# Performance work log

Measured on AMD Instinct MI355X. Metric: run time of the kernel, lower is better.

## Reference

```python
import jax, jax.numpy as jnp
import numpy as np

B = 16
COUNTS = np.array([6, 14, 10, 8, 16, 12, 9, 11, 7, 13, 10, 10, 8, 12, 6, 8], dtype=np.int64)  # sum=160, max=16
INPUT_DIM = 1024
D_IN = 834   # num_features_mixed4f + 2
G = 256      # num_features_gcn
NG = 4       # num_graphs
T, H, W = 8, 14, 14


def setup_inputs() -> dict:
    key = jax.random.key(0)
    ks = jax.random.split(key, 7)
    total = int(COUNTS.sum())
    return {
        "actor_features": jax.random.normal(ks[0], (total, INPUT_DIM), dtype=jnp.float32),
        "feature_map": jax.random.normal(ks[1], (B, D_IN, T, H, W), dtype=jnp.float32),
        "W_a": jax.random.normal(ks[2], (NG, G, INPUT_DIM), dtype=jnp.float32) * 0.02,
        "b_a": jnp.zeros((NG, G), dtype=jnp.float32),
        "W_c": jax.random.normal(ks[3], (NG, G, D_IN), dtype=jnp.float32) * 0.02,
        "b_c": jnp.zeros((NG, G), dtype=jnp.float32),
        "W_h": jax.random.normal(ks[4], (NG, G, G), dtype=jnp.float32) * 0.02,
        "num_actors_list": COUNTS,
        "return_features": 0,
    }


def _ragged_indices(counts):
    # static (concrete) ragged bookkeeping
    counts = np.asarray(counts)
    Bn = counts.shape[0]
    Nmax = int(counts.max())
    offsets = np.concatenate([np.zeros(1, np.int64), np.cumsum(counts)[:-1]])
    n = np.arange(Nmax)
    pad_idx = offsets[:, None] + np.minimum(n[None, :], counts[:, None] - 1)  # [B, Nmax]
    valid = (n[None, :] < counts[:, None])                                     # [B, Nmax]
    unpad_b = np.repeat(np.arange(Bn), counts)
    unpad_n = np.concatenate([np.arange(c) for c in counts])
    return pad_idx, valid, unpad_b, unpad_n


def reference(actor_features, feature_map, W_a, b_a, W_c, b_c, W_h,
              num_actors_list, return_features):
    pad_idx, valid, unpad_b, unpad_n = _ragged_indices(num_actors_list)
    valid_f = jnp.asarray(valid, actor_features.dtype)
    Bn = feature_map.shape[0]

    # actor embedding for all graphs: [total, ng, G]
    emb = jnp.einsum('td,gfd->tgf', actor_features, W_a) + b_a[None]
    # pad to [B, Nmax, ng, G]; zero padded slots (matches pad_sequence)
    padded = emb[pad_idx] * valid_f[:, :, None, None]

    # 1x1x1 conv == channel matmul over flattened spatio-temporal grid S=T*H*W
    fm = feature_map.reshape(Bn, feature_map.shape[1], -1)            # [B, C, S]
    ctx = jnp.einsum('bcs,gfc->bgfs', fm, W_c) + b_c[None, :, :, None]  # [B, ng, G, S]

    # adjacency: actor x context similarities, softmax over context locations
    adj = jnp.einsum('bngf,bgfs->bgns', padded, ctx)                  # [B, ng, Nmax, S]
    adj = jax.nn.softmax(adj, axis=-1)
    adj = adj * valid_f[:, None, :, None]                             # masked_fill pad rows -> 0

    # aggregate context + residual
    upd = jnp.einsum('bgns,bgfs->bngf', adj, ctx) + padded            # [B, Nmax, ng, G]

    # unpad back to ragged flat [total, ng, G] (dropout is identity in eval)
    flat = upd[unpad_b, unpad_n]
    out = jax.nn.relu(jnp.einsum('tgf,ghf->tgh', flat, W_h))          # head_linear + relu

    # func == 'concat': cat over graphs along feature dim -> [total, ng*G]
    return out.reshape(out.shape[0], -1)
```

## Files before the change

### kernel.cpp

```cpp
#include <hip/hip_runtime.h>

#define TOTAL   160
#define NMAX    16
#define INDIM   1024
#define DIN     834
#define KPAD    864
#define GF      256
#define SS      1568
#define SPAD    1664
#define CROW    264

__constant__ int c_counts[16] = {6,14,10,8,16,12,9,11,7,13,10,10,8,12,6,8};
__constant__ int c_offs[16]   = {0,6,20,30,38,54,66,75,86,93,106,116,126,134,146,152};
__constant__ int c_t0[8] = {0, 6, 12, 18, 25, 31, 37, 43};
__constant__ int c_t1[8] = {6, 12, 18, 25, 31, 37, 43, 49};

using bf16x8 = __attribute__((ext_vector_type(8))) short;
using f32x4  = __attribute__((ext_vector_type(4))) float;
using us4    = __attribute__((ext_vector_type(4))) unsigned short;

__device__ inline unsigned short f2bf(float f) {
  union { float f; unsigned u; } v; v.f = f;
  const unsigned u = v.u;
  return (unsigned short)((u + 0x7FFFu + ((u >> 16) & 1u)) >> 16);
}
__device__ inline float bf2f(unsigned short h) {
  union { unsigned u; float f; } v; v.u = ((unsigned)h) << 16; return v.f;
}

__global__ __launch_bounds__(256) void prep_all(
    const float* __restrict__ actor, const float* __restrict__ Wa,
    const float* __restrict__ b_a, const float* __restrict__ Wc,
    const float* __restrict__ Wh, const float* __restrict__ fm,
    float* __restrict__ emb, unsigned short* __restrict__ emb_h,
    unsigned short* __restrict__ Ah, unsigned short* __restrict__ Wh_h,
    unsigned short* __restrict__ BhT)
{
  __shared__ float tile[32][33];
  __shared__ unsigned short As[64 * 40];
  __shared__ unsigned short Bs[64 * 40];
  const int bid = blockIdx.x, tid = threadIdx.x;

  if (bid < 48) {
    const int n0 = (bid & 15) * 64, m0 = (bid >> 4) * 64;
    const int wave = tid >> 6, lane = tid & 63;
    const int wm = (wave >> 1) * 32, wn = (wave & 1) * 32;
    const int quad = lane >> 4, lr = lane & 15;
    const int r = tid >> 2, ko = (tid & 3) * 8;
    const bool mval = (m0 + r < TOTAL);

    f32x4 acc[2][2];
    #pragma unroll
    for (int i = 0; i < 2; ++i)
      #pragma unroll
      for (int j = 0; j < 2; ++j) acc[i][j] = (f32x4){0.f, 0.f, 0.f, 0.f};

    const float4 zf4 = {0.f, 0.f, 0.f, 0.f};
    float4 ra0, ra1, rb0, rb1;
    ra0 = mval ? *reinterpret_cast<const float4*>(actor + (size_t)(m0 + r) * INDIM + ko) : zf4;
    ra1 = mval ? *reinterpret_cast<const float4*>(actor + (size_t)(m0 + r) * INDIM + ko + 4) : zf4;
    rb0 = *reinterpret_cast<const float4*>(Wa + (size_t)(n0 + r) * INDIM + ko);
    rb1 = *reinterpret_cast<const float4*>(Wa + (size_t)(n0 + r) * INDIM + ko + 4);

    for (int kt = 0; kt < 32; ++kt) {
      __syncthreads();
      {
        us4 a0, a1, b0, b1;
        a0[0]=f2bf(ra0.x); a0[1]=f2bf(ra0.y); a0[2]=f2bf(ra0.z); a0[3]=f2bf(ra0.w);
        a1[0]=f2bf(ra1.x); a1[1]=f2bf(ra1.y); a1[2]=f2bf(ra1.z); a1[3]=f2bf(ra1.w);
        b0[0]=f2bf(rb0.x); b0[1]=f2bf(rb0.y); b0[2]=f2bf(rb0.z); b0[3]=f2bf(rb0.w);
        b1[0]=f2bf(rb1.x); b1[1]=f2bf(rb1.y); b1[2]=f2bf(rb1.z); b1[3]=f2bf(rb1.w);
        *reinterpret_cast<us4*>(&As[r * 40 + ko])     = a0;
        *reinterpret_cast<us4*>(&As[r * 40 + ko + 4]) = a1;
        *reinterpret_cast<us4*>(&Bs[r * 40 + ko])     = b0;
        *reinterpret_cast<us4*>(&Bs[r * 40 + ko + 4]) = b1;
      }
      __syncthreads();
      if (kt < 31) {
        const int k0 = (kt + 1) * 32;
        ra0 = mval ? *reinterpret_cast<const float4*>(actor + (size_t)(m0 + r) * INDIM + k0 + ko) : zf4;
        ra1 = mval ? *reinterpret_cast<const float4*>(actor + (size_t)(m0 + r) * INDIM + k0 + ko + 4) : zf4;
        rb0 = *reinterpret_cast<const float4*>(Wa + (size_t)(n0 + r) * INDIM + k0 + ko);
        rb1 = *reinterpret_cast<const float4*>(Wa + (size_t)(n0 + r) * INDIM + k0 + ko + 4);
      }
      bf16x8 af[2], bfr[2];
      #pragma unroll
      for (int i = 0; i < 2; ++i)
        af[i] = *reinterpret_cast<const bf16x8*>(&As[(wm + i * 16 + lr) * 40 + quad * 8]);
      #pragma unroll
      for (int j = 0; j < 2; ++j)
        bfr[j] = *reinterpret_cast<const bf16x8*>(&Bs[(wn + j * 16 + lr) * 40 + quad * 8]);
      #pragma unroll
      for (int i = 0; i < 2; ++i)
        #pragma unroll
        for (int j = 0; j < 2; ++j)
          acc[i][j] = __builtin_amdgcn_mfma_f32_16x16x32_bf16(af[i], bfr[j], acc[i][j], 0, 0, 0);
    }

    #pragma unroll
    for (int i = 0; i < 2; ++i) {
      #pragma unroll
      for (int reg = 0; reg < 4; ++reg) {
        const int m = m0 + wm + i * 16 + quad * 4 + reg;
        if (m >= TOTAL) continue;
        #pragma unroll
        for (int j = 0; j < 2; ++j) {
          const int n = n0 + wn + j * 16 + lr;
          const float v = acc[i][j][reg] + b_a[n];
          emb[(size_t)m * INDIM + n] = v;
          emb_h[(size_t)m * INDIM + n] = f2bf(v);
        }
      }
    }
  } else if (bid < 3760) {
    const int pb = bid - 48;
    if (pb < 3456) {
      const int idx = pb * 256 + tid;
      const int k = idx % KPAD, gm = idx / KPAD;
      Ah[idx] = (k < DIN) ? f2bf(Wc[gm * DIN + k]) : (unsigned short)0;
    } else {
      const int i = (pb - 3456) * 256 + tid;
      const float4 v = reinterpret_cast<const float4*>(Wh)[i];
      us4 o; o[0] = f2bf(v.x); o[1] = f2bf(v.y); o[2] = f2bf(v.z); o[3] = f2bf(v.w);
      reinterpret_cast<us4*>(Wh_h)[i] = o;
    }
  } else {
    const int fb = bid - 3760;
    const int sx = fb % 49, ky = (fb / 49) % 27, b = fb / (49 * 27);
    const int k0 = ky * 32, s0 = sx * 32;
    const int tx = tid & 31, ty = tid >> 5;
    const float* src = fm + (size_t)b * DIN * SS;
    #pragma unroll
    for (int r = 0; r < 4; ++r) {
      const int k = k0 + ty + r * 8;
      tile[ty + r * 8][tx] = (k < DIN) ? src[(size_t)k * SS + s0 + tx] : 0.f;
    }
    __syncthreads();
    unsigned short* dst = BhT + (size_t)b * SS * KPAD;
    #pragma unroll
    for (int r = 0; r < 4; ++r) {
      const int s = s0 + ty + r * 8;
      dst[(size_t)s * KPAD + k0 + tx] = f2bf(tile[tx][ty + r * 8]);
    }
  }
}

#define CTX_STEP(RA0, RA1, RB0, RB1, KT)                                               \
  {                                                                                    \
    __syncthreads();                                                                   \
    *reinterpret_cast<uint4*>(&As[r0 * 40 + ko0]) = RA0;                               \
    *reinterpret_cast<uint4*>(&As[r1 * 40 + ko1]) = RA1;                               \
    *reinterpret_cast<uint4*>(&Bs[r0 * 40 + ko0]) = RB0;                               \
    *reinterpret_cast<uint4*>(&Bs[r1 * 40 + ko1]) = RB1;                               \
    __syncthreads();                                                                   \
    if ((KT) + 2 < 27) {                                                               \
      const int k0n = ((KT) + 2) * 32;                                                 \
      RA0 = *reinterpret_cast<const uint4*>(Ag + (size_t)(m0 + r0) * KPAD + k0n + ko0);\
      RA1 = *reinterpret_cast<const uint4*>(Ag + (size_t)(m0 + r1) * KPAD + k0n + ko1);\
      RB0 = *reinterpret_cast<const uint4*>(Bg + (size_t)r0 * KPAD + k0n + ko0);       \
      RB1 = *reinterpret_cast<const uint4*>(Bg + (size_t)r1 * KPAD + k0n + ko1);       \
    }                                                                                  \
    bf16x8 af[4], bfr[4];                                                              \
    _Pragma("unroll")                                                                  \
    for (int i = 0; i < 4; ++i)                                                        \
      af[i] = *reinterpret_cast<const bf16x8*>(&As[(wm + i * 16 + lr) * 40 + quad * 8]); \
    _Pragma("unroll")                                                                  \
    for (int j = 0; j < 4; ++j)                                                        \
      bfr[j] = *reinterpret_cast<const bf16x8*>(&Bs[(wn + j * 16 + lr) * 40 + quad * 8]); \
    _Pragma("unroll")                                                                  \
    for (int i = 0; i < 4; ++i)                                                        \
      _Pragma("unroll")                                                                \
      for (int j = 0; j < 4; ++j)                                                      \
        acc[i][j] = __builtin_amdgcn_mfma_f32_16x16x32_bf16(af[i], bfr[j], acc[i][j], 0, 0, 0); \
  }

__global__ __launch_bounds__(256, 3) void ctx_mfma(const unsigned short* __restrict__ Ah,
                                                   const unsigned short* __restrict__ BhT,
                                                   const float* __restrict__ b_c,
                                                   unsigned short* __restrict__ ctxT) {
  __shared__ unsigned short As[128 * 40];
  __shared__ unsigned short Bs[128 * 40];
  const int zb = blockIdx.z;
  const int g = zb & 3, b = zb >> 2;
  const int zout = (g << 4) + b;
  const int n0 = blockIdx.x * 128;
  const int m0 = blockIdx.y * 128;
  const int tid = threadIdx.x;
  const int wave = tid >> 6, lane = tid & 63;
  const int wm = (wave >> 1) * 64, wn = (wave & 1) * 64;
  const int quad = lane >> 4, lr = lane & 15;

  const unsigned short* Ag = BhT + (size_t)b * SS * KPAD;
  const unsigned short* Bg = Ah + (size_t)g * 256 * KPAD + (size_t)n0 * KPAD;

  const int c0 = tid, c1 = tid + 256;
  const int r0 = c0 >> 2, ko0 = (c0 & 3) * 8;
  const int r1 = c1 >> 2, ko1 = (c1 & 3) * 8;

  f32x4 acc[4][4];
  #pragma unroll
  for (int i = 0; i < 4; ++i)
    #pragma unroll
    for (int j = 0; j < 4; ++j) acc[i][j] = (f32x4){0.f, 0.f, 0.f, 0.f};

  uint4 ra0a, ra1a, rb0a, rb1a, ra0b, ra1b, rb0b, rb1b;
  ra0a = *reinterpret_cast<const uint4*>(Ag + (size_t)(m0 + r0) * KPAD + ko0);
  ra1a = *reinterpret_cast<const uint4*>(Ag + (size_t)(m0 + r1) * KPAD + ko1);
  rb0a = *reinterpret_cast<const uint4*>(Bg + (size_t)r0 * KPAD + ko0);
  rb1a = *reinterpret_cast<const uint4*>(Bg + (size_t)r1 * KPAD + ko1);
  ra0b = *reinterpret_cast<const uint4*>(Ag + (size_t)(m0 + r0) * KPAD + 32 + ko0);
  ra1b = *reinterpret_cast<const uint4*>(Ag + (size_t)(m0 + r1) * KPAD + 32 + ko1);
  rb0b = *reinterpret_cast<const uint4*>(Bg + (size_t)r0 * KPAD + 32 + ko0);
  rb1b = *reinterpret_cast<const uint4*>(Bg + (size_t)r1 * KPAD + 32 + ko1);

  for (int kt = 0; kt < 27; kt += 2) {
    CTX_STEP(ra0a, ra1a, rb0a, rb1a, kt);
    if (kt + 1 < 27) CTX_STEP(ra0b, ra1b, rb0b, rb1b, kt + 1);
  }

  unsigned short* Cz = ctxT + (size_t)zout * SPAD * GF;
  const float* bias = b_c + g * GF;
  #pragma unroll
  for (int j = 0; j < 4; ++j) {
    const int n = n0 + wn + j * 16 + lr;
    const float bv = bias[n];
    #pragma unroll
    for (int i = 0; i < 4; ++i) {
      #pragma unroll
      for (int reg = 0; reg < 4; ++reg) {
        const int m = m0 + wm + i * 16 + quad * 4 + reg;
        Cz[(size_t)m * GF + n] = f2bf(acc[i][j][reg] + bv);
      }
    }
  }
}

__global__ __launch_bounds__(256) void att_part(
    const unsigned short* __restrict__ ctxT,
    const unsigned short* __restrict__ emb_h,
    float* __restrict__ Opart,
    float* __restrict__ Spart)
{
  __shared__ unsigned short Cs[4][32 * CROW];
  __shared__ float Ps[4][32][20];
  __shared__ float walpha[4][16];
  __shared__ float wms[4][16], wls[4][16];
  const int sc = blockIdx.x, z = blockIdx.y;
  const int g = z >> 4, b = z & 15;
  const int count = c_counts[b], off = c_offs[b];
  const int t0 = c_t0[sc], t1 = c_t1[sc];
  const int tid = threadIdx.x, wave = tid >> 6, lane = tid & 63;
  const int quad = lane >> 4, lr = lane & 15;
  const unsigned short* Az = ctxT + (size_t)z * SPAD * GF;
  const bool bvalid = (lr < count);
  const unsigned short* Brow = emb_h + (size_t)(off + (bvalid ? lr : 0)) * INDIM + (g << 8);
  unsigned short* myC = &Cs[wave][0];
  const int fbase = quad * 64 + lr * 4;
  const bf16x8 zero8 = (bf16x8)(short)0;

  float O[16][4];
  #pragma unroll
  for (int n = 0; n < 16; ++n)
    #pragma unroll
    for (int j = 0; j < 4; ++j) O[n][j] = 0.f;
  float m_run = -3.0e38f, l_run = 0.f;

  for (int t = t0 + wave; t < t1; t += 4) {
    const int s0 = t * 32;
    #pragma unroll
    for (int q = 0; q < 16; ++q) {
      const int row = 2 * q + (lane >> 5);
      const int col = (lane & 31) * 8;
      const uint4 v = *reinterpret_cast<const uint4*>(Az + (size_t)(s0 + row) * GF + col);
      *reinterpret_cast<uint4*>(&myC[row * CROW + col]) = v;
    }
    f32x4 acc[2] = {(f32x4){0.f,0.f,0.f,0.f}, (f32x4){0.f,0.f,0.f,0.f}};
    #pragma unroll
    for (int kk = 0; kk < 8; ++kk) {
      const int f = kk * 32 + quad * 8;
      bf16x8 bv8 = *reinterpret_cast<const bf16x8*>(Brow + f);
      if (!bvalid) bv8 = zero8;
      #pragma unroll
      for (int i = 0; i < 2; ++i) {
        const bf16x8 av8 = *reinterpret_cast<const bf16x8*>(&myC[(i * 16 + lr) * CROW + f]);
        acc[i] = __builtin_amdgcn_mfma_f32_16x16x32_bf16(av8, bv8, acc[i], 0, 0, 0);
      }
    }
    float mx = acc[0][0];
    #pragma unroll
    for (int i = 0; i < 2; ++i)
      #pragma unroll
      for (int r = 0; r < 4; ++r) mx = fmaxf(mx, acc[i][r]);
    float lsum = 0.f;
    #pragma unroll
    for (int i = 0; i < 2; ++i)
      #pragma unroll
      for (int r = 0; r < 4; ++r) lsum += __expf(acc[i][r] - mx);
    #pragma unroll
    for (int d = 16; d < 64; d <<= 1) {
      const float om = __shfl_xor(mx, d, 64);
      const float ol = __shfl_xor(lsum, d, 64);
      const float M = fmaxf(mx, om);
      lsum = lsum * __expf(mx - M) + ol * __expf(om - M);
      mx = M;
    }
    const float m_new = fmaxf(m_run, mx);
    const float alpha = __expf(m_run - m_new);
    const float beta  = __expf(mx - m_new);
    l_run = alpha * l_run + beta * lsum;
    m_run = m_new;
    if (lane < 16) walpha[wave][lane] = alpha;
    #pragma unroll
    for (int i = 0; i < 2; ++i)
      #pragma unroll
      for (int r = 0; r < 4; ++r) {
        const int sl = i * 16 + quad * 4 + r;
        Ps[wave][sl][lr] = beta * __expf(acc[i][r] - mx);
      }
    float av[16];
    {
      const float4 a0 = *reinterpret_cast<const float4*>(&walpha[wave][0]);
      const float4 a1 = *reinterpret_cast<const float4*>(&walpha[wave][4]);
      const float4 a2 = *reinterpret_cast<const float4*>(&walpha[wave][8]);
      const float4 a3 = *reinterpret_cast<const float4*>(&walpha[wave][12]);
      av[0]=a0.x; av[1]=a0.y; av[2]=a0.z; av[3]=a0.w;
      av[4]=a1.x; av[5]=a1.y; av[6]=a1.z; av[7]=a1.w;
      av[8]=a2.x; av[9]=a2.y; av[10]=a2.z; av[11]=a2.w;
      av[12]=a3.x; av[13]=a3.y; av[14]=a3.z; av[15]=a3.w;
    }
    #pragma unroll
    for (int n = 0; n < 16; ++n)
      #pragma unroll
      for (int j = 0; j < 4; ++j) O[n][j] *= av[n];
    for (int s = 0; s < 32; ++s) {
      const float4 p0 = *reinterpret_cast<const float4*>(&Ps[wave][s][0]);
      const float4 p1 = *reinterpret_cast<const float4*>(&Ps[wave][s][4]);
      const float4 p2 = *reinterpret_cast<const float4*>(&Ps[wave][s][8]);
      const float4 p3 = *reinterpret_cast<const float4*>(&Ps[wave][s][12]);
      const us4 cv = *reinterpret_cast<const us4*>(&myC[s * CROW + fbase]);
      const float c0 = bf2f(cv[0]), c1 = bf2f(cv[1]), c2 = bf2f(cv[2]), c3 = bf2f(cv[3]);
      const float pn[16] = {p0.x,p0.y,p0.z,p0.w, p1.x,p1.y,p1.z,p1.w,
                            p2.x,p2.y,p2.z,p2.w, p3.x,p3.y,p3.z,p3.w};
      #pragma unroll
      for (int n = 0; n < 16; ++n) {
        O[n][0] = fmaf(pn[n], c0, O[n][0]);
        O[n][1] = fmaf(pn[n], c1, O[n][1]);
        O[n][2] = fmaf(pn[n], c2, O[n][2]);
        O[n][3] = fmaf(pn[n], c3, O[n][3]);
      }
    }
  }

  if (lane < 16) { wms[wave][lane] = m_run; wls[wave][lane] = l_run; }
  __syncthreads();
  float* Ob = reinterpret_cast<float*>(&Cs[wave][0]);
  #pragma unroll
  for (int n = 0; n < 16; ++n) {
    const float Mb = fmaxf(fmaxf(wms[0][n], wms[1][n]), fmaxf(wms[2][n], wms[3][n]));
    const float e = __expf(wms[wave][n] - Mb);
    #pragma unroll
    for (int j = 0; j < 4; ++j) Ob[n * 256 + fbase + j] = O[n][j] * e;
  }
  __syncthreads();
  float* Op = Opart + ((size_t)z * 8 + sc) * 4096;
  #pragma unroll
  for (int nn = 0; nn < 4; ++nn) {
    const int n = wave * 4 + nn;
    float4 v = {0.f, 0.f, 0.f, 0.f};
    #pragma unroll
    for (int w = 0; w < 4; ++w) {
      const float4 x = *reinterpret_cast<const float4*>(
          reinterpret_cast<const float*>(&Cs[w][0]) + n * 256 + fbase);
      v.x += x.x; v.y += x.y; v.z += x.z; v.w += x.w;
    }
    *reinterpret_cast<float4*>(Op + n * 256 + fbase) = v;
  }
  if (wave == 0 && lane < 16) {
    const int n = lane;
    const float Mb = fmaxf(fmaxf(wms[0][n], wms[1][n]), fmaxf(wms[2][n], wms[3][n]));
    float Lb = 0.f;
    #pragma unroll
    for (int w = 0; w < 4; ++w) Lb += wls[w][n] * __expf(wms[w][n] - Mb);
    Spart[((size_t)z * 8 + sc) * 32 + n]      = Mb;
    Spart[((size_t)z * 8 + sc) * 32 + 16 + n] = Lb;
  }
}

__global__ __launch_bounds__(256) void att_combine(
    const float* __restrict__ Opart, const float* __restrict__ Spart,
    const float* __restrict__ emb, unsigned short* __restrict__ flat_h) {
  const int z = blockIdx.x, n = blockIdx.y;
  const int g = z >> 4, b = z & 15;
  const int count = c_counts[b], off = c_offs[b];
  if (n >= count) return;
  const int f = threadIdx.x;
  float M = -3.0e38f;
  #pragma unroll
  for (int sc = 0; sc < 8; ++sc)
    M = fmaxf(M, Spart[((size_t)z * 8 + sc) * 32 + n]);
  float L = 0.f, acc = 0.f;
  #pragma unroll
  for (int sc = 0; sc < 8; ++sc) {
    const float e = __expf(Spart[((size_t)z * 8 + sc) * 32 + n] - M);
    L += e * Spart[((size_t)z * 8 + sc) * 32 + 16 + n];
    acc += e * Opart[((size_t)z * 8 + sc) * 4096 + n * 256 + f];
  }
  const int t = off + n;
  const int col = (g << 8) + f;
  flat_h[t * INDIM + col] = f2bf(acc / L + emb[t * INDIM + col]);
}

__global__ __launch_bounds__(256) void head_mfma(const unsigned short* __restrict__ flat_h,
                                                 const unsigned short* __restrict__ Wh_h,
                                                 float* __restrict__ out) {
  __shared__ unsigned short As[64 * 40];
  __shared__ unsigned short Bs[64 * 40];
  const int g = blockIdx.z;
  const int n0 = blockIdx.x * 64, m0 = blockIdx.y * 64;
  const int tid = threadIdx.x;
  const int wave = tid >> 6, lane = tid & 63;
  const int wm = (wave >> 1) * 32, wn = (wave & 1) * 32;
  const int quad = lane >> 4, lr = lane & 15;
  const int r = tid >> 2, ko = (tid & 3) * 8;

  const unsigned short* Ag = flat_h + (size_t)m0 * INDIM + g * GF;
  const unsigned short* Bg = Wh_h + (size_t)g * GF * GF + (size_t)n0 * GF;

  f32x4 acc[2][2];
  #pragma unroll
  for (int i = 0; i < 2; ++i)
    #pragma unroll
    for (int j = 0; j < 2; ++j) acc[i][j] = (f32x4){0.f, 0.f, 0.f, 0.f};

  const uint4 zero4 = {0u, 0u, 0u, 0u};
  uint4 ra, rb;
  ra = (m0 + r < TOTAL) ? *reinterpret_cast<const uint4*>(Ag + (size_t)r * INDIM + ko) : zero4;
  rb = *reinterpret_cast<const uint4*>(Bg + (size_t)r * GF + ko);

  for (int kt = 0; kt < 8; ++kt) {
    __syncthreads();
    *reinterpret_cast<uint4*>(&As[r * 40 + ko]) = ra;
    *reinterpret_cast<uint4*>(&Bs[r * 40 + ko]) = rb;
    __syncthreads();
    if (kt < 7) {
      const int k0 = (kt + 1) * 32;
      ra = (m0 + r < TOTAL) ? *reinterpret_cast<const uint4*>(Ag + (size_t)r * INDIM + k0 + ko) : zero4;
      rb = *reinterpret_cast<const uint4*>(Bg + (size_t)r * GF + k0 + ko);
    }
    bf16x8 af[2], bfr[2];
    #pragma unroll
    for (int i = 0; i < 2; ++i)
      af[i] = *reinterpret_cast<const bf16x8*>(&As[(wm + i * 16 + lr) * 40 + quad * 8]);
    #pragma unroll
    for (int j = 0; j < 2; ++j)
      bfr[j] = *reinterpret_cast<const bf16x8*>(&Bs[(wn + j * 16 + lr) * 40 + quad * 8]);
    #pragma unroll
    for (int i = 0; i < 2; ++i)
      #pragma unroll
      for (int j = 0; j < 2; ++j)
        acc[i][j] = __builtin_amdgcn_mfma_f32_16x16x32_bf16(af[i], bfr[j], acc[i][j], 0, 0, 0);
  }

  #pragma unroll
  for (int i = 0; i < 2; ++i) {
    #pragma unroll
    for (int reg = 0; reg < 4; ++reg) {
      const int m = m0 + wm + i * 16 + quad * 4 + reg;
      if (m >= TOTAL) continue;
      #pragma unroll
      for (int j = 0; j < 2; ++j) {
        const int n = n0 + wn + j * 16 + lr;
        out[(size_t)m * INDIM + g * GF + n] = fmaxf(acc[i][j][reg], 0.f);
      }
    }
  }
}

extern "C" void kernel_launch(void* const* d_in, const int* in_sizes, int n_in,
                              void* d_out, int out_size, void* d_ws, size_t ws_size,
                              hipStream_t stream) {
  (void)in_sizes; (void)n_in; (void)out_size; (void)ws_size;
  const float* actor = (const float*)d_in[0];
  const float* fmap  = (const float*)d_in[1];
  const float* W_a   = (const float*)d_in[2];
  const float* b_a   = (const float*)d_in[3];
  const float* W_c   = (const float*)d_in[4];
  const float* b_c   = (const float*)d_in[5];
  const float* W_h   = (const float*)d_in[6];
  float* out = (float*)d_out;
  char* ws = (char*)d_ws;

  float* emb             = (float*)(ws);
  unsigned short* flat_h = (unsigned short*)(ws + 655360);
  unsigned short* emb_h  = (unsigned short*)(ws + 983040);
  float* Spart           = (float*)(ws + 1310720);
  unsigned short* ctxT   = (unsigned short*)(ws + 1376256);
  unsigned short* Ah     = (unsigned short*)(ws + 55902208);
  unsigned short* BhT    = (unsigned short*)(ws + 57671680);
  float* Opart           = (float*)(ws + 57671680);
  unsigned short* Wh_h   = (unsigned short*)(ws + 101023744);

  hipLaunchKernelGGL(prep_all, dim3(24928), dim3(256), 0, stream,
                     actor, W_a, b_a, W_c, W_h, fmap,
                     emb, emb_h, Ah, Wh_h, BhT);

  hipLaunchKernelGGL(ctx_mfma, dim3(2, 13, 64), dim3(256), 0, stream, Ah, BhT, b_c, ctxT);

  hipLaunchKernelGGL(att_part, dim3(8, 64), dim3(256), 0, stream,
                     ctxT, emb_h, Opart, Spart);

  hipLaunchKernelGGL(att_combine, dim3(64, 16), dim3(256), 0, stream,
                     Opart, Spart, emb, flat_h);

  hipLaunchKernelGGL(head_mfma, dim3(4, 3, 4), dim3(256), 0, stream,
                     flat_h, Wh_h, out);
}
```

Baseline: 280.5 us.

## Use direct global-to-LDS loads and XCD-aware block mapping in ctx GEMM

The ctx GEMM now loads its A and B tiles with global_load_lds, which writes straight into shared memory instead of staging through registers. It also drops the register double-buffer prefetch and the padded LDS stride. The 3D grid becomes a 1D grid remapped so that each XCD handles two batches, keeping each batch's BhT slice in one XCD's L2. The trade-off is that loads no longer overlap compute within a block, and the unpadded 32-element LDS rows may cause bank conflicts on the fragment reads.

Result: faster. 265.4 us (-5.4%).

```diff
diff --git a/kernel.cpp b/kernel.cpp
--- a/kernel.cpp
+++ b/kernel.cpp
@@ -26,6 +26,12 @@
 }
 __device__ inline float bf2f(unsigned short h) {
   union { unsigned u; float f; } v; v.u = ((unsigned)h) << 16; return v.f;
+}
+
+__device__ __forceinline__ void gload16(const unsigned short* g, unsigned short* l) {
+  __builtin_amdgcn_global_load_lds(
+      (const __attribute__((address_space(1))) unsigned int*)(g),
+      (__attribute__((address_space(3))) unsigned int*)(l), 16, 0, 0);
 }
 
 __global__ __launch_bounds__(256) void prep_all(
@@ -145,57 +151,39 @@
   }
 }
 
-#define CTX_STEP(RA0, RA1, RB0, RB1, KT)                                               \
-  {                                                                                    \
-    __syncthreads();                                                                   \
-    *reinterpret_cast<uint4*>(&As[r0 * 40 + ko0]) = RA0;                               \
-    *reinterpret_cast<uint4*>(&As[r1 * 40 + ko1]) = RA1;                               \
-    *reinterpret_cast<uint4*>(&Bs[r0 * 40 + ko0]) = RB0;                               \
-    *reinterpret_cast<uint4*>(&Bs[r1 * 40 + ko1]) = RB1;                               \
-    __syncthreads();                                                                   \
-    if ((KT) + 2 < 27) {                                                               \
-      const int k0n = ((KT) + 2) * 32;                                                 \
-      RA0 = *reinterpret_cast<const uint4*>(Ag + (size_t)(m0 + r0) * KPAD + k0n + ko0);\
-      RA1 = *reinterpret_cast<const uint4*>(Ag + (size_t)(m0 + r1) * KPAD + k0n + ko1);\
-      RB0 = *reinterpret_cast<const uint4*>(Bg + (size_t)r0 * KPAD + k0n + ko0);       \
-      RB1 = *reinterpret_cast<const uint4*>(Bg + (size_t)r1 * KPAD + k0n + ko1);       \
-    }                                                                                  \
-    bf16x8 af[4], bfr[4];                                                              \
-    _Pragma("unroll")                                                                  \
-    for (int i = 0; i < 4; ++i)                                                        \
-      af[i] = *reinterpret_cast<const bf16x8*>(&As[(wm + i * 16 + lr) * 40 + quad * 8]); \
-    _Pragma("unroll")                                                                  \
-    for (int j = 0; j < 4; ++j)                                                        \
-      bfr[j] = *reinterpret_cast<const bf16x8*>(&Bs[(wn + j * 16 + lr) * 40 + quad * 8]); \
-    _Pragma("unroll")                                                                  \
-    for (int i = 0; i < 4; ++i)                                                        \
-      _Pragma("unroll")                                                                \
-      for (int j = 0; j < 4; ++j)                                                      \
-        acc[i][j] = __builtin_amdgcn_mfma_f32_16x16x32_bf16(af[i], bfr[j], acc[i][j], 0, 0, 0); \
-  }
-
 __global__ __launch_bounds__(256, 3) void ctx_mfma(const unsigned short* __restrict__ Ah,
                                                    const unsigned short* __restrict__ BhT,
                                                    const float* __restrict__ b_c,
                                                    unsigned short* __restrict__ ctxT) {
-  __shared__ unsigned short As[128 * 40];
-  __shared__ unsigned short Bs[128 * 40];
-  const int zb = blockIdx.z;
-  const int g = zb & 3, b = zb >> 2;
+  __shared__ unsigned short As[128 * 32];
+  __shared__ unsigned short Bs[128 * 32];
+  const int lin  = blockIdx.x;
+  const int xcd  = lin & 7;
+  const int slot = lin >> 3;
+  const int bloc = (slot >= 104) ? 1 : 0;
+  const int within = slot - bloc * 104;
+  const int b  = xcd * 2 + bloc;
+  const int mt = within % 13;
+  const int gn = within / 13;
+  const int g  = gn & 3;
+  const int n0 = (gn >> 2) * 128;
+  const int m0 = mt * 128;
   const int zout = (g << 4) + b;
-  const int n0 = blockIdx.x * 128;
-  const int m0 = blockIdx.y * 128;
+
   const int tid = threadIdx.x;
   const int wave = tid >> 6, lane = tid & 63;
   const int wm = (wave >> 1) * 64, wn = (wave & 1) * 64;
   const int quad = lane >> 4, lr = lane & 15;
 
-  const unsigned short* Ag = BhT + (size_t)b * SS * KPAD;
+  const unsigned short* Ag = BhT + (size_t)b * SS * KPAD + (size_t)m0 * KPAD;
   const unsigned short* Bg = Ah + (size_t)g * 256 * KPAD + (size_t)n0 * KPAD;
 
-  const int c0 = tid, c1 = tid + 256;
-  const int r0 = c0 >> 2, ko0 = (c0 & 3) * 8;
-  const int r1 = c1 >> 2, ko1 = (c1 & 3) * 8;
+  const int srow  = wave * 16 + (lane >> 2);
+  const int skoff = (lane & 3) * 8;
+  unsigned short* ldsA0 = As + (wave * 16) * 32;
+  unsigned short* ldsA1 = As + (64 + wave * 16) * 32;
+  unsigned short* ldsB0 = Bs + (wave * 16) * 32;
+  unsigned short* ldsB1 = Bs + (64 + wave * 16) * 32;
 
   f32x4 acc[4][4];
   #pragma unroll
@@ -203,19 +191,27 @@
     #pragma unroll
     for (int j = 0; j < 4; ++j) acc[i][j] = (f32x4){0.f, 0.f, 0.f, 0.f};
 
-  uint4 ra0a, ra1a, rb0a, rb1a, ra0b, ra1b, rb0b, rb1b;
-  ra0a = *reinterpret_cast<const uint4*>(Ag + (size_t)(m0 + r0) * KPAD + ko0);
-  ra1a = *reinterpret_cast<const uint4*>(Ag + (size_t)(m0 + r1) * KPAD + ko1);
-  rb0a = *reinterpret_cast<const uint4*>(Bg + (size_t)r0 * KPAD + ko0);
-  rb1a = *reinterpret_cast<const uint4*>(Bg + (size_t)r1 * KPAD + ko1);
-  ra0b = *reinterpret_cast<const uint4*>(Ag + (size_t)(m0 + r0) * KPAD + 32 + ko0);
-  ra1b = *reinterpret_cast<const uint4*>(Ag + (size_t)(m0 + r1) * KPAD + 32 + ko1);
-  rb0b = *reinterpret_cast<const uint4*>(Bg + (size_t)r0 * KPAD + 32 + ko0);
-  rb1b = *reinterpret_cast<const uint4*>(Bg + (size_t)r1 * KPAD + 32 + ko1);
-
-  for (int kt = 0; kt < 27; kt += 2) {
-    CTX_STEP(ra0a, ra1a, rb0a, rb1a, kt);
-    if (kt + 1 < 27) CTX_STEP(ra0b, ra1b, rb0b, rb1b, kt + 1);
+  for (int kt = 0; kt < 27; ++kt) {
+    const int k0 = kt * 32 + skoff;
+    gload16(Ag + (size_t)srow * KPAD + k0,        ldsA0);
+    gload16(Ag + (size_t)(srow + 64) * KPAD + k0, ldsA1);
+    gload16(Bg + (size_t)srow * KPAD + k0,        ldsB0);
+    gload16(Bg + (size_t)(srow + 64) * KPAD + k0, ldsB1);
+    __syncthreads();
+
+    bf16x8 af[4], bfr[4];
+    #pragma unroll
+    for (int i = 0; i < 4; ++i)
+      af[i] = *reinterpret_cast<const bf16x8*>(&As[(wm + i * 16 + lr) * 32 + quad * 8]);
+    #pragma unroll
+    for (int j = 0; j < 4; ++j)
+      bfr[j] = *reinterpret_cast<const bf16x8*>(&Bs[(wn + j * 16 + lr) * 32 + quad * 8]);
+    #pragma unroll
+    for (int i = 0; i < 4; ++i)
+      #pragma unroll
+      for (int j = 0; j < 4; ++j)
+        acc[i][j] = __builtin_amdgcn_mfma_f32_16x16x32_bf16(af[i], bfr[j], acc[i][j], 0, 0, 0);
+    __syncthreads();
   }
 
   unsigned short* Cz = ctxT + (size_t)zout * SPAD * GF;
@@ -504,7 +500,7 @@
                      actor, W_a, b_a, W_c, W_h, fmap,
                      emb, emb_h, Ah, Wh_h, BhT);
 
-  hipLaunchKernelGGL(ctx_mfma, dim3(2, 13, 64), dim3(256), 0, stream, Ah, BhT, b_c, ctxT);
+  hipLaunchKernelGGL(ctx_mfma, dim3(1664), dim3(256), 0, stream, Ah, BhT, b_c, ctxT);
 
   hipLaunchKernelGGL(att_part, dim3(8, 64), dim3(256), 0, stream,
                      ctxT, emb_h, Opart, Spart);
```
